# Performance work log

Measured on AMD Instinct MI355X. Metric: run time of the kernel, lower is better.

Reference implementation:

```python
import jax, jax.numpy as jnp
import numpy as np

DIM = 96
HEADS = 6
HEAD_DIM = DIM // HEADS  # 16
WIN = 8
N = WIN * WIN            # 64
C = 4 * DIM              # 384
TABLE = (2 * WIN - 1) ** 2  # 225


def setup_inputs() -> dict:
    key = jax.random.key(0)
    ks = jax.random.split(key, 12)
    B_ = 2048  # num_windows * batch = 1024 * 2
    NW = 1024
    x = jax.random.normal(ks[0], (B_, N, C), dtype=jnp.float32)
    cross_x = jax.random.normal(ks[1], (B_, N, C), dtype=jnp.float32)
    rpi = jax.random.randint(ks[2], (N, N), 0, TABLE)
    mask = jnp.zeros((NW, N, N), dtype=jnp.float32)
    s = 0.02
    Wq = jax.random.normal(ks[3], (C, DIM), dtype=jnp.float32) * s
    bq = jnp.zeros((DIM,), dtype=jnp.float32)
    Wk = jax.random.normal(ks[4], (C, DIM), dtype=jnp.float32) * s
    bk = jnp.zeros((DIM,), dtype=jnp.float32)
    Wv = jax.random.normal(ks[5], (C, C), dtype=jnp.float32) * s
    bv = jnp.zeros((C,), dtype=jnp.float32)
    Wp = jax.random.normal(ks[6], (C, C), dtype=jnp.float32) * s
    bp = jnp.zeros((C,), dtype=jnp.float32)
    rpb_table = jax.random.normal(ks[7], (TABLE, HEADS), dtype=jnp.float32) * 0.02
    return {"x": x, "cross_x": cross_x, "rpi": rpi, "mask": mask,
            "Wq": Wq, "bq": bq, "Wk": Wk, "bk": bk, "Wv": Wv, "bv": bv,
            "Wp": Wp, "bp": bp, "rpb_table": rpb_table}


def reference(x, cross_x, rpi, mask, Wq, bq, Wk, bk, Wv, bv, Wp, bp, rpb_table):
    b_, n, c = x.shape
    scale = HEAD_DIM ** (-0.5)
    # projections: q,k -> dim; v -> c (=4*dim)
    q = (x @ Wq + bq).reshape(b_, n, HEADS, HEAD_DIM).transpose(0, 2, 1, 3)
    k = (cross_x @ Wk + bk).reshape(b_, n, HEADS, HEAD_DIM).transpose(0, 2, 1, 3)
    v = (cross_x @ Wv + bv).reshape(b_, n, HEADS, c // HEADS).transpose(0, 2, 1, 3)
    attn = jnp.einsum('bhnd,bhmd->bhnm', q * scale, k)
    # relative position bias: gather (n*n,) indices -> (n, n, heads) -> (heads, n, n)
    bias = rpb_table[rpi.reshape(-1)].reshape(n, n, HEADS).transpose(2, 0, 1)
    attn = attn + bias[None]
    nw = mask.shape[0]
    attn = attn.reshape(b_ // nw, nw, HEADS, n, n) + mask[None, :, None]
    attn = attn.reshape(b_, HEADS, n, n)
    attn = jax.nn.softmax(attn, axis=-1)
    out = jnp.einsum('bhnm,bhmd->bhnd', attn, v)  # (b_, heads, n, c//heads)
    out = out.transpose(0, 2, 1, 3).reshape(b_, n, c)
    out = out @ Wp + bp
    return out
```

## Files before the change

kernel.cpp:

```cpp
#include <hip/hip_runtime.h>
#include <hip/hip_bf16.h>


typedef __attribute__((ext_vector_type(8))) short short8;
typedef __attribute__((ext_vector_type(4))) float f32x4;

__device__ __forceinline__ f32x4 mfma_b16(short8 a, short8 b, f32x4 c) {
  return __builtin_amdgcn_mfma_f32_16x16x32_bf16(a, b, c, 0, 0, 0);
}

__device__ __forceinline__ unsigned short f2bf(float x) {
  return __builtin_bit_cast(unsigned short, __float2bfloat16(x));
}

__device__ __forceinline__ unsigned pack2(float a, float b) {
  return (unsigned)f2bf(a) | ((unsigned)f2bf(b) << 16);
}

__device__ __forceinline__ void gl_lds16(const char* g, char* l) {
  __builtin_amdgcn_global_load_lds(
      (const __attribute__((address_space(1))) unsigned int*)g,
      (__attribute__((address_space(3))) unsigned int*)l, 16, 0, 0);
}

#define HEADSYNC                                                      \
  asm volatile("s_waitcnt vmcnt(0) lgkmcnt(0)" ::: "memory");         \
  __builtin_amdgcn_sched_barrier(0);                                  \
  __builtin_amdgcn_s_barrier();                                       \
  __builtin_amdgcn_sched_barrier(0)

__global__ void prep_k(const float* __restrict__ Wq, const float* __restrict__ Wk,
                       const float* __restrict__ Wv, const float* __restrict__ Wp,
                       const float* __restrict__ rpb, const int* __restrict__ rpi,
                       const float* __restrict__ bk, const float* __restrict__ bv,
                       unsigned short* __restrict__ Wq_t, unsigned short* __restrict__ Wkv_t,
                       unsigned short* __restrict__ Wp_t, float* __restrict__ bias6,
                       float* __restrict__ bias_kv) {
  const int T0 = 96 * 384, T1 = 480 * 384, T2 = 384 * 384, T3 = 6 * 4096, T4 = 480;
  int total = T0 + T1 + T2 + T3 + T4;
  for (int i = blockIdx.x * blockDim.x + threadIdx.x; i < total;
       i += gridDim.x * blockDim.x) {
    int r = i;
    if (r < T0) {
      int n = r / 384, k = r % 384;
      Wq_t[r] = f2bf(Wq[k * 96 + n]);
    } else if ((r -= T0) < T1) {
      int n = r / 384, k = r % 384;
      Wkv_t[r] = f2bf(n < 96 ? Wk[k * 96 + n] : Wv[k * 384 + (n - 96)]);
    } else if ((r -= T1) < T2) {
      int n = r / 384, k = r % 384;
      Wp_t[r] = f2bf(Wp[k * 384 + n]);
    } else if ((r -= T2) < T3) {
      int h = r >> 12, ij = r & 4095;
      bias6[r] = rpb[rpi[ij] * 6 + h];
    } else {
      r -= T3;
      bias_kv[r] = (r < 96) ? bk[r] : bv[r - 96];
    }
  }
}

template <int A_MODE, int OUT_MODE, int NX>
__global__ __launch_bounds__(256, 4) void gemm3_k(
    const void* __restrict__ Av, const unsigned short* __restrict__ Bt,
    const float* __restrict__ bias, void* __restrict__ Outv,
    unsigned short* __restrict__ k_out, unsigned short* __restrict__ vt_out) {
  __shared__ char lds[40960];
  constexpr int AB[2] = {0, 8192}, BB[2] = {16384, 28672};
  const int tid = threadIdx.x, lane = tid & 63, wid = tid >> 6;
  const int g = blockIdx.x;
  const int lg_id = (g & 7) * (NX * 256) + (g >> 3);
  const int my = lg_id / NX, nx = lg_id - my * NX;
  const int m0 = my * 64, n0 = nx * 96;
  const int wm = (wid >> 1) * 32, wn = (wid & 1) * 48;
  const int lr = lane & 15, lg = lane >> 4;

  float4 areg[4];
  const int ar = tid >> 2, aq = tid & 3;

  auto a_issue_f32 = [&](int kt) {
    const float* A = (const float*)Av + (size_t)(m0 + ar) * 384 + kt * 64 + aq * 16;
#pragma unroll
    for (int p = 0; p < 4; ++p) areg[p] = *reinterpret_cast<const float4*>(A + p * 4);
  };
  auto a_write_f32 = [&](char* Ab) {
    unsigned pk[8];
#pragma unroll
    for (int p = 0; p < 4; ++p) {
      pk[p * 2]     = pack2(areg[p].x, areg[p].y);
      pk[p * 2 + 1] = pack2(areg[p].z, areg[p].w);
    }
    const int c0 = aq * 2;
    *reinterpret_cast<uint4*>(Ab + ar * 128 + ((c0 ^ (ar & 7)) * 16)) =
        make_uint4(pk[0], pk[1], pk[2], pk[3]);
    *reinterpret_cast<uint4*>(Ab + ar * 128 + (((c0 + 1) ^ (ar & 7)) * 16)) =
        make_uint4(pk[4], pk[5], pk[6], pk[7]);
  };
  auto b_issue = [&](int kt, char* Bb) {
#pragma unroll
    for (int j = 0; j < 3; ++j) {
      const int rb = (wid * 3 + j) * 8;
      const int row = rb + (lane >> 3), c = lane & 7;
      gl_lds16((const char*)Bt + (size_t)(n0 + row) * 768 + kt * 128 +
                   ((c ^ (row & 7)) * 16),
               Bb + rb * 128);
    }
  };

  f32x4 acc[2][3];
#pragma unroll
  for (int i = 0; i < 2; ++i)
#pragma unroll
    for (int j = 0; j < 3; ++j) acc[i][j] = (f32x4){0.f, 0.f, 0.f, 0.f};

  a_issue_f32(0);
  a_write_f32(lds + AB[0]);
  b_issue(0, lds + BB[0]);
  __syncthreads();

  int cur = 0;
  for (int kt = 0; kt < 6; ++kt) {
    char* An = lds + AB[cur ^ 1];
    char* Bn = lds + BB[cur ^ 1];
    if (kt < 5) {
      a_issue_f32(kt + 1);
      b_issue(kt + 1, Bn);
    }
    {
      const char* Ab = lds + AB[cur];
      const char* Bb = lds + BB[cur];
#pragma unroll
      for (int ks = 0; ks < 2; ++ks) {
        short8 a[2], b[3];
#pragma unroll
        for (int mf = 0; mf < 2; ++mf) {
          const int row = wm + mf * 16 + lr;
          a[mf] = *reinterpret_cast<const short8*>(
              Ab + row * 128 + (((ks * 4 + lg) ^ (row & 7)) * 16));
        }
#pragma unroll
        for (int nf = 0; nf < 3; ++nf) {
          const int row = wn + nf * 16 + lr;
          b[nf] = *reinterpret_cast<const short8*>(
              Bb + row * 128 + (((ks * 4 + lg) ^ (row & 7)) * 16));
        }
#pragma unroll
        for (int mf = 0; mf < 2; ++mf)
#pragma unroll
          for (int nf = 0; nf < 3; ++nf)
            acc[mf][nf] = mfma_b16(a[mf], b[nf], acc[mf][nf]);
      }
    }
    if (kt < 5) a_write_f32(An);
    __syncthreads();
    cur ^= 1;
  }

  if (OUT_MODE == 0 || (OUT_MODE == 2 && nx == 0)) {
    unsigned short* dst = (OUT_MODE == 0) ? (unsigned short*)Outv : k_out;
#pragma unroll
    for (int mf = 0; mf < 2; ++mf)
#pragma unroll
      for (int nf = 0; nf < 3; ++nf) {
        const int col = wn + nf * 16 + lr;
        const float bb = bias[col];
#pragma unroll
        for (int r = 0; r < 4; ++r) {
          const int row = wm + mf * 16 + lg * 4 + r;
          *reinterpret_cast<unsigned short*>(lds + row * 208 + col * 2) =
              f2bf(acc[mf][nf][r] + bb);
        }
      }
    __syncthreads();
#pragma unroll
    for (int j = 0; j < 3; ++j) {
      const int Lb = (j * 256 + tid) * 16;
      const int row = Lb / 192, inner = Lb % 192;
      *reinterpret_cast<uint4*>((char*)dst + (size_t)(m0 + row) * 192 + inner) =
          *reinterpret_cast<const uint4*>(lds + row * 208 + inner);
    }
  } else {
#pragma unroll
    for (int mf = 0; mf < 2; ++mf)
#pragma unroll
      for (int nf = 0; nf < 3; ++nf) {
        const int dl = wn + nf * 16 + lr;
        const float bb = bias[n0 + dl];
        const int tok0 = wm + mf * 16 + lg * 4;
        *reinterpret_cast<unsigned*>(lds + dl * 144 + tok0 * 2) =
            pack2(acc[mf][nf][0] + bb, acc[mf][nf][1] + bb);
        *reinterpret_cast<unsigned*>(lds + dl * 144 + tok0 * 2 + 4) =
            pack2(acc[mf][nf][2] + bb, acc[mf][nf][3] + bb);
      }
    __syncthreads();
#pragma unroll
    for (int j = 0; j < 3; ++j) {
      const int Lc = j * 256 + tid;
      const int dl = Lc >> 3, c = Lc & 7;
      *reinterpret_cast<uint4*>((char*)vt_out + (size_t)my * 49152 +
                                (size_t)((nx - 1) * 96 + dl) * 128 +
                                ((c ^ (dl & 7)) << 4)) =
          *reinterpret_cast<const uint4*>(lds + dl * 144 + c * 16);
    }
  }
}

__global__ __launch_bounds__(256, 3) void ap_k(
    const unsigned short* __restrict__ q_buf, const unsigned short* __restrict__ k_buf,
    const unsigned short* __restrict__ vt_buf, const float* __restrict__ bias6,
    const float* __restrict__ mask, const unsigned short* __restrict__ Wp_t,
    const float* __restrict__ bp, float* __restrict__ out) {
  __shared__ char lds[49152];
  const int tid = threadIdx.x, lane = tid & 63, wid = tid >> 6;
  const int lr = lane & 15, lg = lane >> 4;
  const int w = blockIdx.x;
  char* Pr = lds + 16384;
  char* Bbase = lds + 24576;
  const char* vsrc = (const char*)vt_buf + (size_t)w * 49152;

  auto b_issue = [&](int nc, int kt, char* Bb) {
#pragma unroll
    for (int j = 0; j < 3; ++j) {
      const int rb = (wid * 3 + j) * 8;
      const int row = rb + (lane >> 3), c = lane & 7;
      gl_lds16((const char*)Wp_t + (size_t)(nc * 96 + row) * 768 + kt * 128 +
                   ((c ^ (row & 7)) * 16),
               Bb + rb * 128);
    }
  };
  auto v_issue = [&](int h, int buf) {
    const char* src = vsrc + h * 8192 + wid * 2048 + lane * 16;
    char* dst = lds + buf * 8192 + wid * 2048;
    gl_lds16(src, dst);
    gl_lds16(src + 1024, dst + 1024);
  };

  v_issue(0, 0);
  b_issue(0, 0, Bbase);
  b_issue(1, 0, Bbase + 12288);
  __syncthreads();

  unsigned stash[48];
  const float* mw = mask + (size_t)(w & 1023) * 4096;
  const int iq = wid * 16 + lr;

#pragma unroll
  for (int h = 0; h < 6; ++h) {
    if (h) { HEADSYNC; }
    if (h < 5) v_issue(h + 1, (h + 1) & 1);

    short8 qa = {0, 0, 0, 0, 0, 0, 0, 0};
    if (lg < 2)
      qa = *reinterpret_cast<const short8*>(
          q_buf + (size_t)(w * 64 + iq) * 96 + h * 16 + lg * 8);
    float sv[4][4];
#pragma unroll
    for (int tj = 0; tj < 4; ++tj) {
      short8 kf = {0, 0, 0, 0, 0, 0, 0, 0};
      if (lg < 2)
        kf = *reinterpret_cast<const short8*>(
            k_buf + (size_t)(w * 64 + tj * 16 + lr) * 96 + h * 16 + lg * 8);
      f32x4 z = {0.f, 0.f, 0.f, 0.f};
      f32x4 s = mfma_b16(kf, qa, z);
      const int j0 = tj * 16 + lg * 4;
      const float4 bi = *reinterpret_cast<const float4*>(bias6 + h * 4096 + iq * 64 + j0);
      const float4 mk = *reinterpret_cast<const float4*>(mw + iq * 64 + j0);
      sv[tj][0] = s[0] * 0.25f + bi.x + mk.x;
      sv[tj][1] = s[1] * 0.25f + bi.y + mk.y;
      sv[tj][2] = s[2] * 0.25f + bi.z + mk.z;
      sv[tj][3] = s[3] * 0.25f + bi.w + mk.w;
    }
    float mx = sv[0][0];
#pragma unroll
    for (int tj = 0; tj < 4; ++tj)
#pragma unroll
      for (int r = 0; r < 4; ++r) mx = fmaxf(mx, sv[tj][r]);
    mx = fmaxf(mx, __shfl_xor(mx, 16));
    mx = fmaxf(mx, __shfl_xor(mx, 32));
    float sum = 0.f;
#pragma unroll
    for (int tj = 0; tj < 4; ++tj)
#pragma unroll
      for (int r = 0; r < 4; ++r) {
        sv[tj][r] = __expf(sv[tj][r] - mx);
        sum += sv[tj][r];
      }
    sum += __shfl_xor(sum, 16);
    sum += __shfl_xor(sum, 32);
    const float inv = 1.0f / sum;
#pragma unroll
    for (int tj = 0; tj < 4; ++tj) {
      const int c = tj * 2 + (lg >> 1);
      uint2 st;
      st.x = pack2(sv[tj][0] * inv, sv[tj][1] * inv);
      st.y = pack2(sv[tj][2] * inv, sv[tj][3] * inv);
      *reinterpret_cast<uint2*>(Pr + iq * 128 + ((c ^ (iq & 7)) << 4) +
                                (lg & 1) * 8) = st;
    }
    short8 pa[2];
#pragma unroll
    for (int ks = 0; ks < 2; ++ks)
      pa[ks] = *reinterpret_cast<const short8*>(
          Pr + iq * 128 + (((ks * 4 + lg) ^ (iq & 7)) << 4));
    __builtin_amdgcn_s_setprio(1);
#pragma unroll
    for (int td = 0; td < 4; ++td) {
      f32x4 o = {0.f, 0.f, 0.f, 0.f};
#pragma unroll
      for (int ks = 0; ks < 2; ++ks) {
        const int dr = td * 16 + lr;
        short8 vb = *reinterpret_cast<const short8*>(
            lds + (h & 1) * 8192 + dr * 128 + (((ks * 4 + lg) ^ (dr & 7)) << 4));
        o = mfma_b16(vb, pa[ks], o);
      }
      stash[h * 8 + td * 2 + 0] = pack2(o[0], o[1]);
      stash[h * 8 + td * 2 + 1] = pack2(o[2], o[3]);
    }
    __builtin_amdgcn_s_setprio(0);
  }

#pragma unroll 1
  for (int P = 0; P < 2; ++P) {
    f32x4 acc[2][6];
#pragma unroll
    for (int i = 0; i < 2; ++i)
#pragma unroll
      for (int j = 0; j < 6; ++j) acc[i][j] = (f32x4){0.f, 0.f, 0.f, 0.f};

#pragma unroll
    for (int kt = 0; kt < 6; ++kt) {
#pragma unroll
      for (int td = 0; td < 4; ++td) {
        uint2 st = make_uint2(stash[kt * 8 + td * 2], stash[kt * 8 + td * 2 + 1]);
        *reinterpret_cast<uint2*>(
            Pr + iq * 128 + (((td * 2 + (lg >> 1)) ^ (iq & 7)) << 4) +
            (lg & 1) * 8) = st;
      }
      short8 a0 = *reinterpret_cast<const short8*>(
          Pr + iq * 128 + (((0 * 4 + lg) ^ (iq & 7)) << 4));
      short8 a1 = *reinterpret_cast<const short8*>(
          Pr + iq * 128 + (((1 * 4 + lg) ^ (iq & 7)) << 4));

#pragma unroll
      for (int ncl = 0; ncl < 2; ++ncl) {
        const int T = P * 12 + kt * 2 + ncl;
        if (T >= 1 && T < 23) {
          const int Tn = T + 1;
          const int Pn = Tn / 12, rem = Tn - Pn * 12;
          b_issue(Pn * 2 + (rem & 1), rem >> 1, Bbase + (Tn & 1) * 12288);
        }
        const char* Bb = Bbase + (T & 1) * 12288;
        __builtin_amdgcn_s_setprio(1);
#pragma unroll
        for (int ks = 0; ks < 2; ++ks) {
          const short8 a = ks ? a1 : a0;
#pragma unroll
          for (int nf = 0; nf < 6; ++nf) {
            const int row = nf * 16 + lr;
            const short8 b = *reinterpret_cast<const short8*>(
                Bb + row * 128 + (((ks * 4 + lg) ^ (row & 7)) * 16));
            acc[ncl][nf] = mfma_b16(a, b, acc[ncl][nf]);
          }
        }
        __builtin_amdgcn_s_setprio(0);
        __syncthreads();
      }
    }
#pragma unroll
    for (int ncl = 0; ncl < 2; ++ncl)
#pragma unroll
      for (int nf = 0; nf < 6; ++nf) {
        const int col = (P * 2 + ncl) * 96 + nf * 16 + lr;
        const float bb = bp[col];
#pragma unroll
        for (int r = 0; r < 4; ++r)
          out[(size_t)(w * 64 + wid * 16 + lg * 4 + r) * 384 + col] =
              acc[ncl][nf][r] + bb;
      }
  }
}

extern "C" void kernel_launch(void* const* d_in, const int* in_sizes, int n_in,
                              void* d_out, int out_size, void* d_ws, size_t ws_size,
                              hipStream_t stream) {
  const float* x    = (const float*)d_in[0];
  const float* cx   = (const float*)d_in[1];
  const int*   rpi  = (const int*)d_in[2];
  const float* mask = (const float*)d_in[3];
  const float* Wq   = (const float*)d_in[4];
  const float* bq   = (const float*)d_in[5];
  const float* Wk   = (const float*)d_in[6];
  const float* bk   = (const float*)d_in[7];
  const float* Wv   = (const float*)d_in[8];
  const float* bv   = (const float*)d_in[9];
  const float* Wp   = (const float*)d_in[10];
  const float* bp   = (const float*)d_in[11];
  const float* rpb  = (const float*)d_in[12];

  char* ws = (char*)d_ws;
  unsigned short* Wq_t   = (unsigned short*)(ws + 0);
  unsigned short* Wkv_t  = (unsigned short*)(ws + 73728);
  unsigned short* Wp_t   = (unsigned short*)(ws + 442368);
  float*          bias6  = (float*)(ws + 737280);
  float*          biaskv = (float*)(ws + 835584);
  const size_t MB = 1u << 20;
  unsigned short* q_buf  = (unsigned short*)(ws + MB);
  unsigned short* k_buf  = (unsigned short*)(ws + MB + 25165824u);
  unsigned short* vt_buf = (unsigned short*)(ws + MB + 50331648u);

  prep_k<<<256, 256, 0, stream>>>(Wq, Wk, Wv, Wp, rpb, rpi, bk, bv,
                                  Wq_t, Wkv_t, Wp_t, bias6, biaskv);
  gemm3_k<0, 0, 1><<<2048, 256, 0, stream>>>(x, Wq_t, bq, q_buf, nullptr, nullptr);
  gemm3_k<0, 2, 5><<<10240, 256, 0, stream>>>(cx, Wkv_t, biaskv, nullptr, k_buf, vt_buf);
  ap_k<<<2048, 256, 0, stream>>>(q_buf, k_buf, vt_buf, bias6, mask, Wp_t, bp,
                                 (float*)d_out);
}
```

Measured before the change: 361.8 us.

## Load all V heads upfront and compute all output columns in one pass

```diff
diff --git a/kernel.cpp b/kernel.cpp
--- a/kernel.cpp
+++ b/kernel.cpp
@@ -22,12 +22,6 @@
       (const __attribute__((address_space(1))) unsigned int*)g,
       (__attribute__((address_space(3))) unsigned int*)l, 16, 0, 0);
 }
-
-#define HEADSYNC                                                      \
-  asm volatile("s_waitcnt vmcnt(0) lgkmcnt(0)" ::: "memory");         \
-  __builtin_amdgcn_sched_barrier(0);                                  \
-  __builtin_amdgcn_s_barrier();                                       \
-  __builtin_amdgcn_sched_barrier(0)
 
 __global__ void prep_k(const float* __restrict__ Wq, const float* __restrict__ Wk,
                        const float* __restrict__ Wv, const float* __restrict__ Wp,
@@ -205,50 +199,30 @@
   }
 }
 
-__global__ __launch_bounds__(256, 3) void ap_k(
+__global__ __launch_bounds__(256, 2) void ap_k(
     const unsigned short* __restrict__ q_buf, const unsigned short* __restrict__ k_buf,
     const unsigned short* __restrict__ vt_buf, const float* __restrict__ bias6,
     const float* __restrict__ mask, const unsigned short* __restrict__ Wp_t,
     const float* __restrict__ bp, float* __restrict__ out) {
-  __shared__ char lds[49152];
+  __shared__ char lds[57344];
   const int tid = threadIdx.x, lane = tid & 63, wid = tid >> 6;
   const int lr = lane & 15, lg = lane >> 4;
   const int w = blockIdx.x;
-  char* Pr = lds + 16384;
-  char* Bbase = lds + 24576;
+  char* Pr = lds + 49152;
+
   const char* vsrc = (const char*)vt_buf + (size_t)w * 49152;
-
-  auto b_issue = [&](int nc, int kt, char* Bb) {
-#pragma unroll
-    for (int j = 0; j < 3; ++j) {
-      const int rb = (wid * 3 + j) * 8;
-      const int row = rb + (lane >> 3), c = lane & 7;
-      gl_lds16((const char*)Wp_t + (size_t)(nc * 96 + row) * 768 + kt * 128 +
-                   ((c ^ (row & 7)) * 16),
-               Bb + rb * 128);
-    }
-  };
-  auto v_issue = [&](int h, int buf) {
-    const char* src = vsrc + h * 8192 + wid * 2048 + lane * 16;
-    char* dst = lds + buf * 8192 + wid * 2048;
-    gl_lds16(src, dst);
-    gl_lds16(src + 1024, dst + 1024);
-  };
-
-  v_issue(0, 0);
-  b_issue(0, 0, Bbase);
-  b_issue(1, 0, Bbase + 12288);
+#pragma unroll
+  for (int j = 0; j < 12; ++j) {
+    const int off = (wid * 12 + j) * 1024;
+    gl_lds16(vsrc + off + lane * 16, lds + off);
+  }
   __syncthreads();
 
   unsigned stash[48];
   const float* mw = mask + (size_t)(w & 1023) * 4096;
   const int iq = wid * 16 + lr;
 
-#pragma unroll
   for (int h = 0; h < 6; ++h) {
-    if (h) { HEADSYNC; }
-    if (h < 5) v_issue(h + 1, (h + 1) & 1);
-
     short8 qa = {0, 0, 0, 0, 0, 0, 0, 0};
     if (lg < 2)
       qa = *reinterpret_cast<const short8*>(
@@ -308,9 +282,9 @@
       f32x4 o = {0.f, 0.f, 0.f, 0.f};
 #pragma unroll
       for (int ks = 0; ks < 2; ++ks) {
-        const int dr = td * 16 + lr;
+        const int d = h * 64 + td * 16 + lr;
         short8 vb = *reinterpret_cast<const short8*>(
-            lds + (h & 1) * 8192 + dr * 128 + (((ks * 4 + lg) ^ (dr & 7)) << 4));
+            lds + d * 128 + (((ks * 4 + lg) ^ (d & 7)) << 4));
         o = mfma_b16(vb, pa[ks], o);
       }
       stash[h * 8 + td * 2 + 0] = pack2(o[0], o[1]);
@@ -318,66 +292,67 @@
     }
     __builtin_amdgcn_s_setprio(0);
   }
+  __syncthreads();
+
+  f32x4 acc[4][6];
+#pragma unroll
+  for (int i = 0; i < 4; ++i)
+#pragma unroll
+    for (int j = 0; j < 6; ++j) acc[i][j] = (f32x4){0.f, 0.f, 0.f, 0.f};
 
 #pragma unroll 1
-  for (int P = 0; P < 2; ++P) {
-    f32x4 acc[2][6];
-#pragma unroll
-    for (int i = 0; i < 2; ++i)
-#pragma unroll
-      for (int j = 0; j < 6; ++j) acc[i][j] = (f32x4){0.f, 0.f, 0.f, 0.f};
-
-#pragma unroll
-    for (int kt = 0; kt < 6; ++kt) {
-#pragma unroll
-      for (int td = 0; td < 4; ++td) {
-        uint2 st = make_uint2(stash[kt * 8 + td * 2], stash[kt * 8 + td * 2 + 1]);
-        *reinterpret_cast<uint2*>(
-            Pr + iq * 128 + (((td * 2 + (lg >> 1)) ^ (iq & 7)) << 4) +
-            (lg & 1) * 8) = st;
-      }
-      short8 a0 = *reinterpret_cast<const short8*>(
-          Pr + iq * 128 + (((0 * 4 + lg) ^ (iq & 7)) << 4));
-      short8 a1 = *reinterpret_cast<const short8*>(
-          Pr + iq * 128 + (((1 * 4 + lg) ^ (iq & 7)) << 4));
-
-#pragma unroll
-      for (int ncl = 0; ncl < 2; ++ncl) {
-        const int T = P * 12 + kt * 2 + ncl;
-        if (T >= 1 && T < 23) {
-          const int Tn = T + 1;
-          const int Pn = Tn / 12, rem = Tn - Pn * 12;
-          b_issue(Pn * 2 + (rem & 1), rem >> 1, Bbase + (Tn & 1) * 12288);
+  for (int kt = 0; kt < 6; ++kt) {
+#pragma unroll
+    for (int t = 0; t < 4; ++t)
+#pragma unroll
+      for (int j = 0; j < 3; ++j) {
+        const int rb = (wid * 3 + j) * 8;
+        const int row = rb + (lane >> 3), c = lane & 7;
+        gl_lds16((const char*)Wp_t + (size_t)(t * 96 + row) * 768 + kt * 128 +
+                     ((c ^ (row & 7)) * 16),
+                 lds + t * 12288 + rb * 128);
+      }
+#pragma unroll
+    for (int td = 0; td < 4; ++td) {
+      uint2 st = make_uint2(stash[kt * 8 + td * 2], stash[kt * 8 + td * 2 + 1]);
+      *reinterpret_cast<uint2*>(
+          Pr + iq * 128 + (((td * 2 + (lg >> 1)) ^ (iq & 7)) << 4) +
+          (lg & 1) * 8) = st;
+    }
+    short8 a0 = *reinterpret_cast<const short8*>(
+        Pr + iq * 128 + (((0 * 4 + lg) ^ (iq & 7)) << 4));
+    short8 a1 = *reinterpret_cast<const short8*>(
+        Pr + iq * 128 + (((1 * 4 + lg) ^ (iq & 7)) << 4));
+    __syncthreads();
+    __builtin_amdgcn_s_setprio(1);
+#pragma unroll
+    for (int t = 0; t < 4; ++t)
+#pragma unroll
+      for (int ks = 0; ks < 2; ++ks) {
+        const short8 a = ks ? a1 : a0;
+#pragma unroll
+        for (int nf = 0; nf < 6; ++nf) {
+          const int row = nf * 16 + lr;
+          const short8 b = *reinterpret_cast<const short8*>(
+              lds + t * 12288 + row * 128 + (((ks * 4 + lg) ^ (row & 7)) * 16));
+          acc[t][nf] = mfma_b16(a, b, acc[t][nf]);
         }
-        const char* Bb = Bbase + (T & 1) * 12288;
-        __builtin_amdgcn_s_setprio(1);
-#pragma unroll
-        for (int ks = 0; ks < 2; ++ks) {
-          const short8 a = ks ? a1 : a0;
-#pragma unroll
-          for (int nf = 0; nf < 6; ++nf) {
-            const int row = nf * 16 + lr;
-            const short8 b = *reinterpret_cast<const short8*>(
-                Bb + row * 128 + (((ks * 4 + lg) ^ (row & 7)) * 16));
-            acc[ncl][nf] = mfma_b16(a, b, acc[ncl][nf]);
-          }
-        }
-        __builtin_amdgcn_s_setprio(0);
-        __syncthreads();
-      }
-    }
-#pragma unroll
-    for (int ncl = 0; ncl < 2; ++ncl)
-#pragma unroll
-      for (int nf = 0; nf < 6; ++nf) {
-        const int col = (P * 2 + ncl) * 96 + nf * 16 + lr;
-        const float bb = bp[col];
-#pragma unroll
-        for (int r = 0; r < 4; ++r)
-          out[(size_t)(w * 64 + wid * 16 + lg * 4 + r) * 384 + col] =
-              acc[ncl][nf][r] + bb;
-      }
-  }
+      }
+    __builtin_amdgcn_s_setprio(0);
+    __syncthreads();
+  }
+
+#pragma unroll
+  for (int t = 0; t < 4; ++t)
+#pragma unroll
+    for (int nf = 0; nf < 6; ++nf) {
+      const int col = t * 96 + nf * 16 + lr;
+      const float bb = bp[col];
+#pragma unroll
+      for (int r = 0; r < 4; ++r)
+        out[(size_t)(w * 64 + wid * 16 + lg * 4 + r) * 384 + col] =
+            acc[t][nf][r] + bb;
+    }
 }
 
 extern "C" void kernel_launch(void* const* d_in, const int* in_sizes, int n_in,
```

After: 378.5 us. 1.05x slower.
